# Optimization experiments

Hardware: AMD Instinct MI355X
Metric: run time of the kernel (lower is better)

The kernel has to match this reference:

```python
import jax, jax.numpy as jnp
import numpy as np
import math

CLASSES = 1024
IN_F = 32
OUT_F = 32
N = 262144


def setup_inputs() -> dict:
    key = jax.random.key(0)
    k1, k2, k3, k4 = jax.random.split(key, 4)
    k = math.sqrt(1.0 / float(IN_F))
    inp = jax.random.normal(k1, (N, IN_F), dtype=jnp.float32)
    inds = jax.random.randint(k2, (N,), 0, CLASSES, dtype=jnp.int32)
    w = jax.random.uniform(k3, (CLASSES, IN_F, OUT_F), dtype=jnp.float32, minval=-k, maxval=k)
    b = jax.random.uniform(k4, (CLASSES, 1, OUT_F), dtype=jnp.float32, minval=-k, maxval=k)
    return {"input": inp, "inds": inds, "w": w, "b": b}


def reference(input, inds, w, b):
    # per-row expert matmul: out[n] = input[n] @ w[inds[n]] + b[inds[n]]
    w_g = w[inds]            # [n, in, out] gathered expert weights
    b_g = b[inds, 0]         # [n, out]
    return jnp.einsum('ni,nio->no', input, w_g) + b_g
```

## Files before the change

### kernel.cpp

```cpp
#include <hip/hip_runtime.h>


#define N_ROWS      262144
#define N_CLASSES   1024
#define IN_F        32
#define OUT_F       32
#define HIST_BLOCKS 64
#define ROWS_PER_HB (N_ROWS / HIST_BLOCKS)

__global__ __launch_bounds__(256) void k_hist(const int* __restrict__ inds,
                                              int* __restrict__ bc) {
    __shared__ int h[N_CLASSES];
    const int tid = threadIdx.x;
    for (int c = tid; c < N_CLASSES; c += 256) h[c] = 0;
    __syncthreads();
    const int base = blockIdx.x * ROWS_PER_HB;
    for (int k = 0; k < ROWS_PER_HB; k += 256) {
        int c = inds[base + k + tid];
        atomicAdd(&h[c], 1);
    }
    __syncthreads();
    for (int c = tid; c < N_CLASSES; c += 256)
        bc[blockIdx.x * N_CLASSES + c] = h[c];
}

__global__ __launch_bounds__(1024) void k_scan(int* __restrict__ bc,
                                               int* __restrict__ cls_off) {
    __shared__ int s[N_CLASSES];
    const int c = threadIdx.x;
    int total = 0;
    for (int b = 0; b < HIST_BLOCKS; ++b) total += bc[b * N_CLASSES + c];
    s[c] = total;
    __syncthreads();
    for (int off = 1; off < N_CLASSES; off <<= 1) {
        int v = (c >= off) ? s[c - off] : 0;
        __syncthreads();
        s[c] += v;
        __syncthreads();
    }
    const int base = s[c] - total;
    cls_off[c] = base;
    if (c == N_CLASSES - 1) cls_off[N_CLASSES] = s[c];
    int run = base;
    for (int b = 0; b < HIST_BLOCKS; ++b) {
        int t = bc[b * N_CLASSES + c];
        bc[b * N_CLASSES + c] = run;
        run += t;
    }
}

__global__ __launch_bounds__(256) void k_scatter(const int* __restrict__ inds,
                                                 const int* __restrict__ bc,
                                                 int* __restrict__ rowids) {
    __shared__ int cur[N_CLASSES];
    const int tid = threadIdx.x;
    for (int c = tid; c < N_CLASSES; c += 256)
        cur[c] = bc[blockIdx.x * N_CLASSES + c];
    __syncthreads();
    const int base = blockIdx.x * ROWS_PER_HB;
    for (int k = 0; k < ROWS_PER_HB; k += 256) {
        int row = base + k + tid;
        int c = inds[row];
        int pos = atomicAdd(&cur[c], 1);
        rowids[pos] = row;
    }
}

__global__ __launch_bounds__(256) void k_condmul(const float* __restrict__ input,
                                                 const float* __restrict__ w,
                                                 const float* __restrict__ bias,
                                                 const int* __restrict__ rowids,
                                                 const int* __restrict__ cls_off,
                                                 float* __restrict__ out) {
    __shared__ float wlds[IN_F * OUT_F];
    const int cls = blockIdx.x;
    const int tid = threadIdx.x;

    ((float4*)wlds)[tid] = ((const float4*)(w + (size_t)cls * IN_F * OUT_F))[tid];

    const int oq = tid & 7;
    const int rg = tid >> 3;
    const float4 bv = ((const float4*)(bias + (size_t)cls * OUT_F))[oq];
    const int start = cls_off[cls];
    const int count = cls_off[cls + 1] - start;
    __syncthreads();

    const float4* wl4 = (const float4*)wlds;
    const int iters = (count + 31) >> 5;
    for (int it = 0; it < iters; ++it) {
        const int ri = it * 32 + rg;
        const bool valid = ri < count;
        const int idx = valid ? ri : (count - 1);
        const int row = rowids[start + idx];

        const float4* xin = (const float4*)(input + (size_t)row * IN_F);
        float4 x[8];
#pragma unroll
        for (int j = 0; j < 8; ++j) x[j] = xin[j];

        float4 acc = bv;
#pragma unroll
        for (int j = 0; j < 8; ++j) {
            const float a0 = x[j].x, a1 = x[j].y, a2 = x[j].z, a3 = x[j].w;
            const float4 w0 = wl4[(j * 4 + 0) * (OUT_F / 4) + oq];
            const float4 w1 = wl4[(j * 4 + 1) * (OUT_F / 4) + oq];
            const float4 w2 = wl4[(j * 4 + 2) * (OUT_F / 4) + oq];
            const float4 w3 = wl4[(j * 4 + 3) * (OUT_F / 4) + oq];
            acc.x += a0 * w0.x; acc.y += a0 * w0.y; acc.z += a0 * w0.z; acc.w += a0 * w0.w;
            acc.x += a1 * w1.x; acc.y += a1 * w1.y; acc.z += a1 * w1.z; acc.w += a1 * w1.w;
            acc.x += a2 * w2.x; acc.y += a2 * w2.y; acc.z += a2 * w2.z; acc.w += a2 * w2.w;
            acc.x += a3 * w3.x; acc.y += a3 * w3.y; acc.z += a3 * w3.z; acc.w += a3 * w3.w;
        }
        if (valid)
            ((float4*)(out + (size_t)row * OUT_F))[oq] = acc;
    }
}

__global__ __launch_bounds__(256) void k_naive(const float* __restrict__ input,
                                               const int* __restrict__ inds,
                                               const float* __restrict__ w,
                                               const float* __restrict__ bias,
                                               float* __restrict__ out) {
    const int tid = threadIdx.x;
    const int oq = tid & 7;
    const int rg = tid >> 3;
    const int row = blockIdx.x * 32 + rg;
    if (row >= N_ROWS) return;
    const int c = inds[row];
    const float4* xin = (const float4*)(input + (size_t)row * IN_F);
    const float4* wr = (const float4*)(w + (size_t)c * IN_F * OUT_F);
    float4 acc = ((const float4*)(bias + (size_t)c * OUT_F))[oq];
#pragma unroll
    for (int j = 0; j < 8; ++j) {
        const float4 xv = xin[j];
        const float a0 = xv.x, a1 = xv.y, a2 = xv.z, a3 = xv.w;
        const float4 w0 = wr[(j * 4 + 0) * (OUT_F / 4) + oq];
        const float4 w1 = wr[(j * 4 + 1) * (OUT_F / 4) + oq];
        const float4 w2 = wr[(j * 4 + 2) * (OUT_F / 4) + oq];
        const float4 w3 = wr[(j * 4 + 3) * (OUT_F / 4) + oq];
        acc.x += a0 * w0.x; acc.y += a0 * w0.y; acc.z += a0 * w0.z; acc.w += a0 * w0.w;
        acc.x += a1 * w1.x; acc.y += a1 * w1.y; acc.z += a1 * w1.z; acc.w += a1 * w1.w;
        acc.x += a2 * w2.x; acc.y += a2 * w2.y; acc.z += a2 * w2.z; acc.w += a2 * w2.w;
        acc.x += a3 * w3.x; acc.y += a3 * w3.y; acc.z += a3 * w3.z; acc.w += a3 * w3.w;
    }
    ((float4*)(out + (size_t)row * OUT_F))[oq] = acc;
}

extern "C" void kernel_launch(void* const* d_in, const int* in_sizes, int n_in,
                              void* d_out, int out_size, void* d_ws, size_t ws_size,
                              hipStream_t stream) {
    const float* input = (const float*)d_in[0];
    const int*   inds  = (const int*)d_in[1];
    const float* w     = (const float*)d_in[2];
    const float* bias  = (const float*)d_in[3];
    float* out = (float*)d_out;

    int* ws = (int*)d_ws;
    int* bc      = ws;
    int* cls_off = ws + HIST_BLOCKS * N_CLASSES;
    int* rowids  = cls_off + N_CLASSES + 1 + 3;
    const size_t need = (size_t)(HIST_BLOCKS * N_CLASSES + N_CLASSES + 4 + N_ROWS) * sizeof(int);

    if (ws_size >= need) {
        k_hist<<<HIST_BLOCKS, 256, 0, stream>>>(inds, bc);
        k_scan<<<1, 1024, 0, stream>>>(bc, cls_off);
        k_scatter<<<HIST_BLOCKS, 256, 0, stream>>>(inds, bc, rowids);
        k_condmul<<<N_CLASSES, 256, 0, stream>>>(input, w, bias, rowids, cls_off, out);
    } else {
        k_naive<<<N_ROWS / 32, 256, 0, stream>>>(input, inds, w, bias, out);
    }
}
```

Before: 121.4 us.

## Use global atomic histogram and scatter, register-block four rows per thread

Replaces the per-block histogram matrix and serial 64-step per-class scan with global atomic class counts, a simple 1024-wide scan that also initializes per-class cursors, and a fully parallel scatter with one thread per row using global atomics. The expert matmul now processes four rows per thread per iteration, so each LDS weight load is reused across four rows and more global loads are in flight. The aim is to shorten the serial scan and scatter stages and raise ILP in the matmul. The cost is global atomic contention in the scatter, a nondeterministic row order within each class, and higher register pressure.

```diff
diff --git a/kernel.cpp b/kernel.cpp
--- a/kernel.cpp
+++ b/kernel.cpp
@@ -9,74 +9,61 @@
 #define ROWS_PER_HB (N_ROWS / HIST_BLOCKS)
 
 __global__ __launch_bounds__(256) void k_hist(const int* __restrict__ inds,
-                                              int* __restrict__ bc) {
+                                              int* __restrict__ cnt) {
     __shared__ int h[N_CLASSES];
     const int tid = threadIdx.x;
     for (int c = tid; c < N_CLASSES; c += 256) h[c] = 0;
     __syncthreads();
     const int base = blockIdx.x * ROWS_PER_HB;
-    for (int k = 0; k < ROWS_PER_HB; k += 256) {
-        int c = inds[base + k + tid];
-        atomicAdd(&h[c], 1);
-    }
+    for (int k = 0; k < ROWS_PER_HB; k += 256)
+        atomicAdd(&h[inds[base + k + tid]], 1);
     __syncthreads();
-    for (int c = tid; c < N_CLASSES; c += 256)
-        bc[blockIdx.x * N_CLASSES + c] = h[c];
-}
-
-__global__ __launch_bounds__(1024) void k_scan(int* __restrict__ bc,
-                                               int* __restrict__ cls_off) {
-    __shared__ int s[N_CLASSES];
-    const int c = threadIdx.x;
-    int total = 0;
-    for (int b = 0; b < HIST_BLOCKS; ++b) total += bc[b * N_CLASSES + c];
-    s[c] = total;
-    __syncthreads();
-    for (int off = 1; off < N_CLASSES; off <<= 1) {
-        int v = (c >= off) ? s[c - off] : 0;
-        __syncthreads();
-        s[c] += v;
-        __syncthreads();
-    }
-    const int base = s[c] - total;
-    cls_off[c] = base;
-    if (c == N_CLASSES - 1) cls_off[N_CLASSES] = s[c];
-    int run = base;
-    for (int b = 0; b < HIST_BLOCKS; ++b) {
-        int t = bc[b * N_CLASSES + c];
-        bc[b * N_CLASSES + c] = run;
-        run += t;
+    for (int c = tid; c < N_CLASSES; c += 256) {
+        int v = h[c];
+        if (v) atomicAdd(&cnt[c], v);
     }
 }
 
-__global__ __launch_bounds__(256) void k_scatter(const int* __restrict__ inds,
-                                                 const int* __restrict__ bc,
-                                                 int* __restrict__ rowids) {
-    __shared__ int cur[N_CLASSES];
-    const int tid = threadIdx.x;
-    for (int c = tid; c < N_CLASSES; c += 256)
-        cur[c] = bc[blockIdx.x * N_CLASSES + c];
+__global__ __launch_bounds__(1024) void k_scan(const int* __restrict__ cnt,
+                                               int* __restrict__ cls_off,
+                                               int* __restrict__ cursor) {
+    __shared__ int s[N_CLASSES];
+    const int c = threadIdx.x;
+    const int v = cnt[c];
+    s[c] = v;
     __syncthreads();
-    const int base = blockIdx.x * ROWS_PER_HB;
-    for (int k = 0; k < ROWS_PER_HB; k += 256) {
-        int row = base + k + tid;
-        int c = inds[row];
-        int pos = atomicAdd(&cur[c], 1);
-        rowids[pos] = row;
+    for (int off = 1; off < N_CLASSES; off <<= 1) {
+        int t = (c >= off) ? s[c - off] : 0;
+        __syncthreads();
+        s[c] += t;
+        __syncthreads();
     }
+    const int excl = s[c] - v;
+    cls_off[c] = excl;
+    cursor[c] = excl;
+    if (c == N_CLASSES - 1) cls_off[N_CLASSES] = s[c];
 }
 
-__global__ __launch_bounds__(256) void k_condmul(const float* __restrict__ input,
+__global__ __launch_bounds__(256) void k_scatter(const int* __restrict__ inds,
+                                                 int* __restrict__ cursor,
+                                                 int* __restrict__ rowids) {
+    const int row = blockIdx.x * 256 + threadIdx.x;
+    const int c = inds[row];
+    const int pos = atomicAdd(&cursor[c], 1);
+    rowids[pos] = row;
+}
+
+__global__ __launch_bounds__(256) void k_condmul(const float4* __restrict__ input4,
                                                  const float* __restrict__ w,
                                                  const float* __restrict__ bias,
                                                  const int* __restrict__ rowids,
                                                  const int* __restrict__ cls_off,
-                                                 float* __restrict__ out) {
-    __shared__ float wlds[IN_F * OUT_F];
+                                                 float4* __restrict__ out4) {
+    __shared__ float4 wlds4[IN_F * 8];
     const int cls = blockIdx.x;
     const int tid = threadIdx.x;
 
-    ((float4*)wlds)[tid] = ((const float4*)(w + (size_t)cls * IN_F * OUT_F))[tid];
+    wlds4[tid] = ((const float4*)(w + (size_t)cls * IN_F * OUT_F))[tid];
 
     const int oq = tid & 7;
     const int rg = tid >> 3;
@@ -84,35 +71,48 @@
     const int start = cls_off[cls];
     const int count = cls_off[cls + 1] - start;
     __syncthreads();
+    if (count == 0) return;
 
-    const float4* wl4 = (const float4*)wlds;
-    const int iters = (count + 31) >> 5;
+    const int iters = (count + 127) >> 7;
     for (int it = 0; it < iters; ++it) {
-        const int ri = it * 32 + rg;
-        const bool valid = ri < count;
-        const int idx = valid ? ri : (count - 1);
-        const int row = rowids[start + idx];
+        const int rbase = it * 128 + rg * 4;
+        int rows[4];
+        bool val[4];
+#pragma unroll
+        for (int r = 0; r < 4; ++r) {
+            const int ri = rbase + r;
+            val[r] = ri < count;
+            rows[r] = rowids[start + (val[r] ? ri : 0)];
+        }
+        float4 x[4][8];
+#pragma unroll
+        for (int r = 0; r < 4; ++r)
+#pragma unroll
+            for (int j = 0; j < 8; ++j)
+                x[r][j] = input4[(size_t)rows[r] * 8 + j];
 
-        const float4* xin = (const float4*)(input + (size_t)row * IN_F);
-        float4 x[8];
-#pragma unroll
-        for (int j = 0; j < 8; ++j) x[j] = xin[j];
-
-        float4 acc = bv;
+        float4 acc[4] = {bv, bv, bv, bv};
 #pragma unroll
         for (int j = 0; j < 8; ++j) {
-            const float a0 = x[j].x, a1 = x[j].y, a2 = x[j].z, a3 = x[j].w;
-            const float4 w0 = wl4[(j * 4 + 0) * (OUT_F / 4) + oq];
-            const float4 w1 = wl4[(j * 4 + 1) * (OUT_F / 4) + oq];
-            const float4 w2 = wl4[(j * 4 + 2) * (OUT_F / 4) + oq];
-            const float4 w3 = wl4[(j * 4 + 3) * (OUT_F / 4) + oq];
-            acc.x += a0 * w0.x; acc.y += a0 * w0.y; acc.z += a0 * w0.z; acc.w += a0 * w0.w;
-            acc.x += a1 * w1.x; acc.y += a1 * w1.y; acc.z += a1 * w1.z; acc.w += a1 * w1.w;
-            acc.x += a2 * w2.x; acc.y += a2 * w2.y; acc.z += a2 * w2.z; acc.w += a2 * w2.w;
-            acc.x += a3 * w3.x; acc.y += a3 * w3.y; acc.z += a3 * w3.z; acc.w += a3 * w3.w;
+#pragma unroll
+            for (int s = 0; s < 4; ++s) {
+                const float4 wk = wlds4[(j * 4 + s) * 8 + oq];
+#pragma unroll
+                for (int r = 0; r < 4; ++r) {
+                    const float xs = (s == 0) ? x[r][j].x
+                                   : (s == 1) ? x[r][j].y
+                                   : (s == 2) ? x[r][j].z
+                                              : x[r][j].w;
+                    acc[r].x += xs * wk.x;
+                    acc[r].y += xs * wk.y;
+                    acc[r].z += xs * wk.z;
+                    acc[r].w += xs * wk.w;
+                }
+            }
         }
-        if (valid)
-            ((float4*)(out + (size_t)row * OUT_F))[oq] = acc;
+#pragma unroll
+        for (int r = 0; r < 4; ++r)
+            if (val[r]) out4[(size_t)rows[r] * 8 + oq] = acc[r];
     }
 }
 
@@ -156,16 +156,19 @@
     float* out = (float*)d_out;
 
     int* ws = (int*)d_ws;
-    int* bc      = ws;
-    int* cls_off = ws + HIST_BLOCKS * N_CLASSES;
-    int* rowids  = cls_off + N_CLASSES + 1 + 3;
-    const size_t need = (size_t)(HIST_BLOCKS * N_CLASSES + N_CLASSES + 4 + N_ROWS) * sizeof(int);
+    int* cnt     = ws;
+    int* cls_off = cnt + N_CLASSES;
+    int* cursor  = cls_off + N_CLASSES + 1 + 3;
+    int* rowids  = cursor + N_CLASSES;
+    const size_t need = (size_t)(N_CLASSES + N_CLASSES + 4 + N_CLASSES + N_ROWS) * sizeof(int);
 
     if (ws_size >= need) {
-        k_hist<<<HIST_BLOCKS, 256, 0, stream>>>(inds, bc);
-        k_scan<<<1, 1024, 0, stream>>>(bc, cls_off);
-        k_scatter<<<HIST_BLOCKS, 256, 0, stream>>>(inds, bc, rowids);
-        k_condmul<<<N_CLASSES, 256, 0, stream>>>(input, w, bias, rowids, cls_off, out);
+        hipMemsetAsync(cnt, 0, N_CLASSES * sizeof(int), stream);
+        k_hist<<<HIST_BLOCKS, 256, 0, stream>>>(inds, cnt);
+        k_scan<<<1, 1024, 0, stream>>>(cnt, cls_off, cursor);
+        k_scatter<<<N_ROWS / 256, 256, 0, stream>>>(inds, cursor, rowids);
+        k_condmul<<<N_CLASSES, 256, 0, stream>>>((const float4*)input, w, bias,
+                                                 rowids, cls_off, (float4*)out);
     } else {
         k_naive<<<N_ROWS / 32, 256, 0, stream>>>(input, inds, w, bias, out);
     }
```

Result: slower. 184.9 us (+52.3%).
